# Kernel tuning notes

Measured on AMD Instinct MI355X. Metric: run time of the kernel, lower is better.

## Reference

```python
import jax, jax.numpy as jnp
import numpy as np

NUM_HEADS = 8

def setup_inputs() -> dict:
    key = jax.random.key(0)
    k0, k1, k2, k3 = jax.random.split(key, 4)
    B, C, H, W = 2, 512, 64, 64
    x = jax.random.normal(k0, (B, C, H, W), dtype=jnp.float32)
    # binary ROI mask (hard mode): 1 inside region, 0 outside
    mask = (jax.random.uniform(k1, (B, 1, H, W)) > 0.5).astype(jnp.float32)
    Wqkv = jax.random.normal(k2, (3 * C, C), dtype=jnp.float32) * 0.02
    bqkv = jnp.zeros((3 * C,), dtype=jnp.float32)
    Wproj = jax.random.normal(k3, (C, C), dtype=jnp.float32) * 0.02
    bproj = jnp.zeros((C,), dtype=jnp.float32)
    return {"x": x, "mask": mask, "Wqkv": Wqkv, "bqkv": bqkv, "Wproj": Wproj, "bproj": bproj}


def reference(x, mask, Wqkv, bqkv, Wproj, bproj):
    B, C, H, W = x.shape
    N = H * W
    d = C // NUM_HEADS
    scale = d ** (-0.5)

    xf = x.reshape(B, C, N)
    # 1x1 conv == per-pixel linear: [3C,C] @ [B,C,N]
    qkv = jnp.einsum('oc,bcn->bon', Wqkv, xf) + bqkv[None, :, None]
    q, k, v = jnp.split(qkv, 3, axis=1)  # each [B,C,N]

    def to_heads(t):  # [B,C,N] -> [B,h,N,d]
        return t.reshape(B, NUM_HEADS, d, N).transpose(0, 1, 3, 2)

    q, k, v = to_heads(q), to_heads(k), to_heads(v)

    attn = jnp.einsum('bhnd,bhmd->bhnm', q, k) * scale  # [B,h,N,N]
    # hard mask bias: -10000 on keys outside ROI, broadcast over query dim
    roi = mask.reshape(B, 1, 1, N)
    attn = attn + (1.0 - roi) * (-10000.0)
    attn = jax.nn.softmax(attn, axis=-1)
    # attn_drop = 0.0 -> identity

    out = jnp.einsum('bhnm,bhmd->bhnd', attn, v)  # [B,h,N,d]
    out = out.transpose(0, 1, 3, 2).reshape(B, C, N)
    out = jnp.einsum('oc,bcn->bon', Wproj, out) + bproj[None, :, None]
    return out.reshape(B, C, H, W)
```

## Files before the change

### kernel.cpp

```cpp
#include <hip/hip_runtime.h>

#define BB 2
#define CC 512
#define NH 8
#define DDIM 64
#define NN 4096
#define QSCALE 0.18033688011112042f
#define MBIAS  -14426.950408889634f

typedef __bf16 bfx8 __attribute__((ext_vector_type(8)));
typedef __bf16 bf2  __attribute__((ext_vector_type(2)));
typedef float  f32x4 __attribute__((ext_vector_type(4)));
typedef int    i32x4 __attribute__((ext_vector_type(4)));
typedef ushort usx8  __attribute__((ext_vector_type(8)));

__device__ inline ushort f2bf(float f) {
  return __builtin_bit_cast(ushort, (__bf16)f);
}
__device__ inline float bf2f(ushort u) {
  return (float)__builtin_bit_cast(__bf16, u);
}

__device__ __forceinline__ void gload_lds16(const void* g, void* l) {
  __builtin_amdgcn_global_load_lds(
      (const __attribute__((address_space(1))) void*)g,
      (__attribute__((address_space(3))) void*)l, 16, 0, 0);
}

__device__ __forceinline__ void swap32(int& a, int& b) {
  asm("v_permlane32_swap_b32 %0, %1" : "+v"(a), "+v"(b));
}
__device__ __forceinline__ void swap16(int& a, int& b) {
  asm("v_permlane16_swap_b32 %0, %1" : "+v"(a), "+v"(b));
}

__global__ __launch_bounds__(256)
void convert_w(const float* __restrict__ Wqkv, const float* __restrict__ Wproj,
               ushort* __restrict__ Wq, ushort* __restrict__ Wp) {
    const int n1 = (1536*CC)/4;
    const int n2 = (CC*CC)/4;
    int i = blockIdx.x*256 + threadIdx.x;
    if (i < n1) {
        float4 v = *(const float4*)(&Wqkv[(size_t)i*4]);
        if (i < 65536) { v.x*=QSCALE; v.y*=QSCALE; v.z*=QSCALE; v.w*=QSCALE; }
        ushort4 o; o.x=f2bf(v.x); o.y=f2bf(v.y); o.z=f2bf(v.z); o.w=f2bf(v.w);
        *(ushort4*)(&Wq[(size_t)i*4]) = o;
    } else if (i < n1+n2) {
        int j = i - n1;
        float4 v = *(const float4*)(&Wproj[(size_t)j*4]);
        ushort4 o; o.x=f2bf(v.x); o.y=f2bf(v.y); o.z=f2bf(v.z); o.w=f2bf(v.w);
        *(ushort4*)(&Wp[(size_t)j*4]) = o;
    }
}

__global__ __launch_bounds__(256)
void transpose_x(const float* __restrict__ x, ushort* __restrict__ xT) {
    const int bn = blockIdx.x, bc = blockIdx.y, b = blockIdx.z;
    const int t = threadIdx.x;
    __shared__ float T[64][65];
    const int n0 = bn*64, c0 = bc*64;
    const int tc = t >> 4, tn4 = (t & 15) * 4;
    #pragma unroll
    for (int r = 0; r < 4; ++r) {
        int c = tc + r*16;
        float4 v = *(const float4*)(&x[((size_t)b*CC + c0 + c)*NN + n0 + tn4]);
        T[c][tn4+0] = v.x; T[c][tn4+1] = v.y; T[c][tn4+2] = v.z; T[c][tn4+3] = v.w;
    }
    __syncthreads();
    #pragma unroll
    for (int r = 0; r < 4; ++r) {
        int n = tc + r*16;
        ushort4 o;
        o.x = f2bf(T[tn4+0][n]); o.y = f2bf(T[tn4+1][n]);
        o.z = f2bf(T[tn4+2][n]); o.w = f2bf(T[tn4+3][n]);
        *(ushort4*)(&xT[((size_t)b*NN + n0 + n)*CC + c0 + tn4]) = o;
    }
}

__global__ __launch_bounds__(256)
void qkv_mfma(const ushort* __restrict__ xT, const ushort* __restrict__ Wb,
              const float* __restrict__ bias, ushort* __restrict__ qws,
              ushort* __restrict__ kws, ushort* __restrict__ vws) {
    const int bn = blockIdx.x;
    const int bo = blockIdx.y;
    const int b  = blockIdx.z;
    const int t  = threadIdx.x;
    const int w  = t >> 6, l = t & 63, g = l >> 4, m = l & 15;
    const int o0 = bo * 128, n0 = bn * 128;
    const int part = o0 >> 9;
    const int wr = w >> 1, wc = w & 1;

    __shared__ __align__(16) ushort SH[2*128*64];
    ushort* Xs  = SH;
    ushort* Ws_ = SH + 128*64;

    const ushort* xbase = xT + ((size_t)b*NN + n0)*CC;
    const ushort* wbase = Wb + (size_t)o0*CC;

    f32x4 acc[4][4];
    #pragma unroll
    for (int i=0;i<4;i++)
        #pragma unroll
        for (int j=0;j<4;j++) acc[i][j] = (f32x4){0.f,0.f,0.f,0.f};

    const ushort* R = (part < 2) ? Xs  : Ws_;
    const ushort* Cc = (part < 2) ? Ws_ : Xs;

    for (int k0 = 0; k0 < CC; k0 += 64) {
        #pragma unroll
        for (int it = 0; it < 4; ++it) {
            int c16 = (it*4 + w)*64 + l;
            int row = c16 >> 3;
            int gch = (c16 & 7) ^ (row & 7);
            gload_lds16(xbase + (size_t)row*CC + k0 + gch*8, Xs  + c16*8);
            gload_lds16(wbase + (size_t)row*CC + k0 + gch*8, Ws_ + c16*8);
        }
        __syncthreads();
        __builtin_amdgcn_s_setprio(1);
        #pragma unroll
        for (int kc = 0; kc < 2; ++kc) {
            bfx8 ra[4], cb[4];
            #pragma unroll
            for (int f = 0; f < 4; ++f) {
                int rrow = wr*64 + f*16 + m;
                ra[f] = *(const bfx8*)(R  + (rrow*8 + ((kc*4+g) ^ (rrow&7)))*8);
                int crow = wc*64 + f*16 + m;
                cb[f] = *(const bfx8*)(Cc + (crow*8 + ((kc*4+g) ^ (crow&7)))*8);
            }
            #pragma unroll
            for (int i = 0; i < 4; ++i)
                #pragma unroll
                for (int j = 0; j < 4; ++j)
                    acc[i][j] = __builtin_amdgcn_mfma_f32_16x16x32_bf16(ra[i], cb[j], acc[i][j], 0, 0, 0);
        }
        __builtin_amdgcn_s_setprio(0);
        __syncthreads();
    }

    float bvj[4];
    float bvi[4][4];
    if (part < 2) {
        const float bs = (part == 0) ? QSCALE : 1.f;
        #pragma unroll
        for (int j = 0; j < 4; ++j) bvj[j] = bias[o0 + wc*64 + j*16 + m] * bs;
    } else {
        #pragma unroll
        for (int i = 0; i < 4; ++i) {
            const float4 bt = *(const float4*)(&bias[o0 + wr*64 + i*16 + g*4]);
            bvi[i][0]=bt.x; bvi[i][1]=bt.y; bvi[i][2]=bt.z; bvi[i][3]=bt.w;
        }
    }
    ushort* Lb = SH;
    #pragma unroll
    for (int i = 0; i < 4; ++i)
        #pragma unroll
        for (int j = 0; j < 4; ++j)
            #pragma unroll
            for (int r = 0; r < 4; ++r) {
                int A = wr*64 + i*16 + g*4 + r;
                int Bc = wc*64 + j*16 + m;
                float val = acc[i][j][r] + ((part < 2) ? bvj[j] : bvi[i][r]);
                int ch = (Bc >> 3) ^ (A & 15);
                Lb[A*128 + ch*8 + (Bc & 7)] = f2bf(val);
            }
    __syncthreads();
    {
        const int row = t >> 1, cp = t & 1;
        const int h0 = (o0 & 511) >> 6;
        ushort* dp;
        if (part < 2) {
            ushort* dst = (part == 0) ? qws : kws;
            dp = dst + (((size_t)b*NH + h0 + cp)*NN + n0 + row)*DDIM;
        } else {
            int h = h0 + (row >> 6), d = row & 63;
            dp = vws + (((size_t)b*NH + h)*DDIM + d)*NN + n0 + cp*64;
        }
        #pragma unroll
        for (int k = 0; k < 8; ++k) {
            int ch = (cp*8 + k) ^ (row & 15);
            *(float4*)(dp + k*8) = *(const float4*)(&Lb[row*128 + ch*8]);
        }
    }
}

__global__ __launch_bounds__(256, 4)
void attn_mfma(const ushort* __restrict__ qw, const ushort* __restrict__ kw,
               const ushort* __restrict__ vw, const float* __restrict__ mask,
               ushort* __restrict__ opart, float* __restrict__ lpart) {
    const int qt = blockIdx.x >> 1, half = blockIdx.x & 1;
    const int h = blockIdx.y, b = blockIdx.z;
    const int t = threadIdx.x;
    const int w = t >> 6, l = t & 63, g = l >> 4, m = l & 15;
    const int n0 = qt * 128;
    const int koff0 = half * 2048;
    const size_t bh = (size_t)b * NH + h;
    const ushort* qp = qw + bh * (size_t)NN * DDIM;
    const ushort* kp = kw + bh * (size_t)NN * DDIM;
    const ushort* vp = vw + bh * (size_t)DDIM * NN;

    __shared__ __align__(16) ushort Ks[2][64*64];
    __shared__ __align__(16) ushort Vs[2][64*64];
    __shared__ float mb[2][64];

    #define STAGE(buf, ko) { \
        _Pragma("unroll") \
        for (int it = 0; it < 2; ++it) { \
            int c16 = it*256 + t; \
            int row = c16 >> 3, gch = (c16 & 7) ^ (row & 7); \
            gload_lds16(kp + (size_t)((ko) + row)*DDIM + gch*8, &Ks[buf][c16*8]); \
            gload_lds16(vp + (size_t)row*NN + (ko) + gch*8, &Vs[buf][c16*8]); \
        } }

    bfx8 qf[2][2];
    #pragma unroll
    for (int qi = 0; qi < 2; ++qi)
        #pragma unroll
        for (int kc = 0; kc < 2; ++kc)
            qf[qi][kc] = *(const bfx8*)(qp + (size_t)(n0 + w*32 + qi*16 + m)*DDIM + kc*32 + g*8);

    f32x4 o[2][4];
    #pragma unroll
    for (int qi=0; qi<2; ++qi)
        #pragma unroll
        for (int f=0; f<4; ++f) o[qi][f] = (f32x4){0.f,0.f,0.f,0.f};
    float l_part[2] = {0.f, 0.f};

    STAGE(0, koff0);
    float mreg = 0.f;
    if (t < 64) mreg = mask[(size_t)b*NN + koff0 + t];
    if (t < 64) mb[0][t] = (1.f - mreg) * MBIAS;
    if (t < 64) mreg = mask[(size_t)b*NN + koff0 + 64 + t];
    __syncthreads();

    for (int kt = 0; kt < 32; ++kt) {
        const int cur = kt & 1, nxt = cur ^ 1;
        if (kt + 1 < 32) {
            STAGE(nxt, koff0 + (kt+1)*64);
            if (t < 64) mb[nxt][t] = (1.f - mreg) * MBIAS;
            if (kt + 2 < 32 && t < 64) mreg = mask[(size_t)b*NN + koff0 + (kt+2)*64 + t];
        }

        float4 mbv[4];
        #pragma unroll
        for (int f=0; f<4; ++f) mbv[f] = *(const float4*)(&mb[cur][f*16 + 4*g]);

        f32x4 sa[2][4];
        #pragma unroll
        for (int qi=0; qi<2; ++qi)
            #pragma unroll
            for (int f=0; f<4; ++f)
                sa[qi][f] = (f32x4){mbv[f].x, mbv[f].y, mbv[f].z, mbv[f].w};
        __builtin_amdgcn_s_setprio(1);
        #pragma unroll
        for (int kc=0; kc<2; ++kc)
            #pragma unroll
            for (int f=0; f<4; ++f) {
                int row = f*16 + m;
                bfx8 kf = *(const bfx8*)(&Ks[cur][row*64 + ((kc*32 + g*8) ^ ((row&7)*8))]);
                #pragma unroll
                for (int qi=0; qi<2; ++qi)
                    sa[qi][f] = __builtin_amdgcn_mfma_f32_16x16x32_bf16(kf, qf[qi][kc], sa[qi][f], 0, 0, 0);
            }
        __builtin_amdgcn_s_setprio(0);

        bfx8 pa[2][2];
        #pragma unroll
        for (int qi=0; qi<2; ++qi) {
            float pv_[4][4];
            float tsum = 0.f;
            #pragma unroll
            for (int f=0; f<4; ++f)
                #pragma unroll
                for (int r=0; r<4; ++r) {
                    float p = __builtin_amdgcn_exp2f(sa[qi][f][r]);
                    pv_[f][r] = p;
                    tsum += p;
                }
            l_part[qi] += tsum;

            int u[4][2];
            #pragma unroll
            for (int f=0; f<4; ++f)
                #pragma unroll
                for (int pp=0; pp<2; ++pp) {
                    bf2 tpk = { (__bf16)pv_[f][2*pp], (__bf16)pv_[f][2*pp+1] };
                    u[f][pp] = __builtin_bit_cast(int, tpk);
                }
            #pragma unroll
            for (int pp=0; pp<2; ++pp) { swap32(u[0][pp], u[1][pp]); swap32(u[2][pp], u[3][pp]); }
            #pragma unroll
            for (int pp=0; pp<2; ++pp) { swap16(u[0][pp], u[1][pp]); swap16(u[2][pp], u[3][pp]); }
            pa[qi][0] = __builtin_bit_cast(bfx8, (i32x4){u[0][0], u[0][1], u[1][0], u[1][1]});
            pa[qi][1] = __builtin_bit_cast(bfx8, (i32x4){u[2][0], u[2][1], u[3][0], u[3][1]});
        }

        __builtin_amdgcn_s_setprio(1);
        #pragma unroll
        for (int kc=0; kc<2; ++kc)
            #pragma unroll
            for (int f=0; f<4; ++f) {
                int row = f*16 + m;
                bfx8 vf = *(const bfx8*)(&Vs[cur][row*64 + ((kc*32 + g*8) ^ ((row&7)*8))]);
                #pragma unroll
                for (int qi=0; qi<2; ++qi)
                    o[qi][f] = __builtin_amdgcn_mfma_f32_16x16x32_bf16(pa[qi][kc], vf, o[qi][f], 0, 0, 0);
            }
        __builtin_amdgcn_s_setprio(0);
        __syncthreads();
    }

    const size_t obase = (bh*2 + half) * (size_t)NN;
    #pragma unroll
    for (int qi=0; qi<2; ++qi) {
        float l_tot = l_part[qi] + __shfl_xor(l_part[qi], 16);
        l_tot += __shfl_xor(l_tot, 32);
        if (g == 0) lpart[obase + n0 + w*32 + qi*16 + m] = l_tot;
        #pragma unroll
        for (int f=0; f<4; ++f)
            #pragma unroll
            for (int r=0; r<4; ++r)
                opart[(obase + n0 + w*32 + qi*16 + 4*g + r)*DDIM + f*16 + m] = f2bf(o[qi][f][r]);
    }
    #undef STAGE
}

__global__ __launch_bounds__(256)
void combine_k(const ushort* __restrict__ opart, const float* __restrict__ lpart,
               ushort* __restrict__ aob) {
    const int t = threadIdx.x;
    const int n = blockIdx.x*64 + (t >> 2), dq = t & 3;
    const int h = blockIdx.y, b = blockIdx.z;
    const size_t bh = (size_t)b*NH + h;
    const float linv = 1.f / (lpart[(bh*2+0)*NN + n] + lpart[(bh*2+1)*NN + n]);
    const ushort* p0 = opart + ((bh*2+0)*(size_t)NN + n)*DDIM + dq*16;
    const ushort* p1 = opart + ((bh*2+1)*(size_t)NN + n)*DDIM + dq*16;
    ushort* dst = aob + ((size_t)b*NN + n)*CC + h*DDIM + dq*16;
    #pragma unroll
    for (int c = 0; c < 2; ++c) {
        usx8 u0 = *(const usx8*)(p0 + c*8);
        usx8 u1 = *(const usx8*)(p1 + c*8);
        usx8 res;
        #pragma unroll
        for (int j = 0; j < 8; ++j)
            res[j] = f2bf((bf2f(u0[j]) + bf2f(u1[j])) * linv);
        *(usx8*)(dst + c*8) = res;
    }
}

__global__ __launch_bounds__(256)
void proj_mfma(const ushort* __restrict__ aob, const ushort* __restrict__ Wp,
               const float* __restrict__ bias, float* __restrict__ out) {
    const int bn = blockIdx.x;
    const int bo = blockIdx.y;
    const int b  = blockIdx.z;
    const int t  = threadIdx.x;
    const int w  = t >> 6, l = t & 63, g = l >> 4, m = l & 15;
    const int o0 = bo * 128, n0 = bn * 128;
    const int wr = w >> 1, wc = w & 1;

    __shared__ __align__(16) ushort As_[128*64];
    __shared__ __align__(16) ushort Ws_[128*64];

    const ushort* abase = aob + ((size_t)b*NN + n0)*CC;
    const ushort* wbase = Wp + (size_t)o0*CC;

    f32x4 acc[4][4];
    #pragma unroll
    for (int i=0;i<4;i++)
        #pragma unroll
        for (int j=0;j<4;j++) acc[i][j] = (f32x4){0.f,0.f,0.f,0.f};

    for (int k0 = 0; k0 < CC; k0 += 64) {
        #pragma unroll
        for (int it = 0; it < 4; ++it) {
            int c16 = (it*4 + w)*64 + l;
            int row = c16 >> 3;
            int gch = (c16 & 7) ^ (row & 7);
            gload_lds16(abase + (size_t)row*CC + k0 + gch*8, As_ + c16*8);
            gload_lds16(wbase + (size_t)row*CC + k0 + gch*8, Ws_ + c16*8);
        }
        __syncthreads();
        __builtin_amdgcn_s_setprio(1);
        #pragma unroll
        for (int kc = 0; kc < 2; ++kc) {
            bfx8 ra[4], cb[4];
            #pragma unroll
            for (int f = 0; f < 4; ++f) {
                int rrow = wr*64 + f*16 + m;
                ra[f] = *(const bfx8*)(Ws_ + (rrow*8 + ((kc*4+g) ^ (rrow&7)))*8);
                int crow = wc*64 + f*16 + m;
                cb[f] = *(const bfx8*)(As_ + (crow*8 + ((kc*4+g) ^ (crow&7)))*8);
            }
            #pragma unroll
            for (int i = 0; i < 4; ++i)
                #pragma unroll
                for (int j = 0; j < 4; ++j)
                    acc[i][j] = __builtin_amdgcn_mfma_f32_16x16x32_bf16(ra[i], cb[j], acc[i][j], 0, 0, 0);
        }
        __builtin_amdgcn_s_setprio(0);
        __syncthreads();
    }
    #pragma unroll
    for (int i = 0; i < 4; ++i)
        #pragma unroll
        for (int r = 0; r < 4; ++r) {
            int o = o0 + wr*64 + i*16 + g*4 + r;
            float bv = bias[o];
            float* dp = out + ((size_t)b*CC + o)*NN;
            #pragma unroll
            for (int j = 0; j < 4; ++j) {
                int n = n0 + wc*64 + j*16 + m;
                dp[n] = acc[i][j][r] + bv;
            }
        }
}

extern "C" void kernel_launch(void* const* d_in, const int* in_sizes, int n_in,
                              void* d_out, int out_size, void* d_ws, size_t ws_size,
                              hipStream_t stream) {
    const float* x     = (const float*)d_in[0];
    const float* mask  = (const float*)d_in[1];
    const float* Wqkv  = (const float*)d_in[2];
    const float* bqkv  = (const float*)d_in[3];
    const float* Wproj = (const float*)d_in[4];
    const float* bproj = (const float*)d_in[5];
    float* out = (float*)d_out;

    const size_t per = (size_t)BB*NH*NN*DDIM;
    ushort* qws = (ushort*)d_ws;
    ushort* kws = qws + per;
    ushort* vws = kws + per;
    ushort* xTb = vws + per;
    ushort* aob = xTb + per;
    ushort* Wqb = aob + per;
    ushort* Wpb = Wqb + (size_t)1536*CC;
    ushort* opart = Wpb + (size_t)CC*CC;
    float*  lpart = (float*)(opart + 2*per);

    convert_w<<<dim3(1024), 256, 0, stream>>>(Wqkv, Wproj, Wqb, Wpb);
    transpose_x<<<dim3(64, 8, BB), 256, 0, stream>>>(x, xTb);
    qkv_mfma<<<dim3(32, 12, BB), 256, 0, stream>>>(xTb, Wqb, bqkv, qws, kws, vws);
    attn_mfma<<<dim3(64, NH, BB), 256, 0, stream>>>(qws, kws, vws, mask, opart, lpart);
    combine_k<<<dim3(64, NH, BB), 256, 0, stream>>>(opart, lpart, aob);
    proj_mfma<<<dim3(32, 4, BB), 256, 0, stream>>>(aob, Wpb, bproj, out);
}
```

Before: 201.7 us.

## Double-buffer GEMM loads, remap blocks across XCDs, precompute mask bias, MFMA row sums

The QKV and projection GEMMs now double-buffer their LDS tiles so the next K-slice loads while the current one computes. All three GEMM-style kernels use a 1D grid with an XCD-aware block remap, which groups blocks that share data onto the same chiplet for L2 reuse. The mask bias is precomputed once in the weight-conversion kernel and read directly from global memory, removing the LDS mask staging. The softmax denominator is now accumulated with an extra MFMA against a ones vector instead of scalar adds and shuffles. The costs are doubled LDS use in the GEMMs, which may lower occupancy, and extra MFMA work in the attention kernel.

```diff
diff --git a/kernel.cpp b/kernel.cpp
--- a/kernel.cpp
+++ b/kernel.cpp
@@ -36,9 +36,12 @@
 
 __global__ __launch_bounds__(256)
 void convert_w(const float* __restrict__ Wqkv, const float* __restrict__ Wproj,
-               ushort* __restrict__ Wq, ushort* __restrict__ Wp) {
+               const float* __restrict__ mask,
+               ushort* __restrict__ Wq, ushort* __restrict__ Wp,
+               float* __restrict__ mbias) {
     const int n1 = (1536*CC)/4;
     const int n2 = (CC*CC)/4;
+    const int n3 = (BB*NN)/4;
     int i = blockIdx.x*256 + threadIdx.x;
     if (i < n1) {
         float4 v = *(const float4*)(&Wqkv[(size_t)i*4]);
@@ -50,6 +53,13 @@
         float4 v = *(const float4*)(&Wproj[(size_t)j*4]);
         ushort4 o; o.x=f2bf(v.x); o.y=f2bf(v.y); o.z=f2bf(v.z); o.w=f2bf(v.w);
         *(ushort4*)(&Wp[(size_t)j*4]) = o;
+    } else if (i < n1+n2+n3) {
+        int j = i - n1 - n2;
+        float4 mv = *(const float4*)(&mask[(size_t)j*4]);
+        float4 ob;
+        ob.x = (1.f - mv.x) * MBIAS; ob.y = (1.f - mv.y) * MBIAS;
+        ob.z = (1.f - mv.z) * MBIAS; ob.w = (1.f - mv.w) * MBIAS;
+        *(float4*)(&mbias[(size_t)j*4]) = ob;
     }
 }
 
@@ -81,18 +91,17 @@
 void qkv_mfma(const ushort* __restrict__ xT, const ushort* __restrict__ Wb,
               const float* __restrict__ bias, ushort* __restrict__ qws,
               ushort* __restrict__ kws, ushort* __restrict__ vws) {
-    const int bn = blockIdx.x;
-    const int bo = blockIdx.y;
-    const int b  = blockIdx.z;
+    const int wg = (blockIdx.x & 7) * 96 + (blockIdx.x >> 3);
+    const int bn = wg & 31;
+    const int bo = (wg % 384) / 32;
+    const int b  = wg / 384;
     const int t  = threadIdx.x;
     const int w  = t >> 6, l = t & 63, g = l >> 4, m = l & 15;
     const int o0 = bo * 128, n0 = bn * 128;
     const int part = o0 >> 9;
     const int wr = w >> 1, wc = w & 1;
 
-    __shared__ __align__(16) ushort SH[2*128*64];
-    ushort* Xs  = SH;
-    ushort* Ws_ = SH + 128*64;
+    __shared__ __align__(16) ushort SH[4*128*64];
 
     const ushort* xbase = xT + ((size_t)b*NN + n0)*CC;
     const ushort* wbase = Wb + (size_t)o0*CC;
@@ -103,19 +112,28 @@
         #pragma unroll
         for (int j=0;j<4;j++) acc[i][j] = (f32x4){0.f,0.f,0.f,0.f};
 
-    const ushort* R = (part < 2) ? Xs  : Ws_;
-    const ushort* Cc = (part < 2) ? Ws_ : Xs;
-
-    for (int k0 = 0; k0 < CC; k0 += 64) {
-        #pragma unroll
-        for (int it = 0; it < 4; ++it) {
-            int c16 = (it*4 + w)*64 + l;
-            int row = c16 >> 3;
-            int gch = (c16 & 7) ^ (row & 7);
-            gload_lds16(xbase + (size_t)row*CC + k0 + gch*8, Xs  + c16*8);
-            gload_lds16(wbase + (size_t)row*CC + k0 + gch*8, Ws_ + c16*8);
-        }
-        __syncthreads();
+    #define QSTAGE(buf, k0) { \
+        _Pragma("unroll") \
+        for (int it = 0; it < 4; ++it) { \
+            int c16 = (it*4 + w)*64 + l; \
+            int row = c16 >> 3; \
+            int gch = (c16 & 7) ^ (row & 7); \
+            gload_lds16(xbase + (size_t)row*CC + (k0) + gch*8, SH + (buf)*8192 + c16*8); \
+            gload_lds16(wbase + (size_t)row*CC + (k0) + gch*8, SH + 16384 + (buf)*8192 + c16*8); \
+        } }
+
+    QSTAGE(0, 0);
+    __syncthreads();
+
+    for (int k0i = 0; k0i < 8; ++k0i) {
+        const int cur = k0i & 1, nxt = cur ^ 1;
+        if (k0i + 1 < 8) QSTAGE(nxt, (k0i+1)*64);
+
+        const ushort* Xs  = SH + cur*8192;
+        const ushort* Ws_ = SH + 16384 + cur*8192;
+        const ushort* R  = (part < 2) ? Xs  : Ws_;
+        const ushort* Cc = (part < 2) ? Ws_ : Xs;
+
         __builtin_amdgcn_s_setprio(1);
         #pragma unroll
         for (int kc = 0; kc < 2; ++kc) {
@@ -136,6 +154,7 @@
         __builtin_amdgcn_s_setprio(0);
         __syncthreads();
     }
+    #undef QSTAGE
 
     float bvj[4];
     float bvi[4][4];
@@ -185,10 +204,11 @@
 
 __global__ __launch_bounds__(256, 4)
 void attn_mfma(const ushort* __restrict__ qw, const ushort* __restrict__ kw,
-               const ushort* __restrict__ vw, const float* __restrict__ mask,
+               const ushort* __restrict__ vw, const float* __restrict__ mbias,
                ushort* __restrict__ opart, float* __restrict__ lpart) {
-    const int qt = blockIdx.x >> 1, half = blockIdx.x & 1;
-    const int h = blockIdx.y, b = blockIdx.z;
+    const int wg = (blockIdx.x & 7) * 128 + (blockIdx.x >> 3);
+    const int qt = (wg & 63) >> 1, half = wg & 1;
+    const int h = (wg >> 6) & 7, b = wg >> 9;
     const int t = threadIdx.x;
     const int w = t >> 6, l = t & 63, g = l >> 4, m = l & 15;
     const int n0 = qt * 128;
@@ -197,10 +217,10 @@
     const ushort* qp = qw + bh * (size_t)NN * DDIM;
     const ushort* kp = kw + bh * (size_t)NN * DDIM;
     const ushort* vp = vw + bh * (size_t)DDIM * NN;
+    const float*  mbp = mbias + (size_t)b*NN + koff0;
 
     __shared__ __align__(16) ushort Ks[2][64*64];
     __shared__ __align__(16) ushort Vs[2][64*64];
-    __shared__ float mb[2][64];
 
     #define STAGE(buf, ko) { \
         _Pragma("unroll") \
@@ -223,33 +243,31 @@
     for (int qi=0; qi<2; ++qi)
         #pragma unroll
         for (int f=0; f<4; ++f) o[qi][f] = (f32x4){0.f,0.f,0.f,0.f};
-    float l_part[2] = {0.f, 0.f};
+    f32x4 lacc[2];
+    lacc[0] = (f32x4){0.f,0.f,0.f,0.f};
+    lacc[1] = (f32x4){0.f,0.f,0.f,0.f};
+    const bfx8 vones = {(__bf16)1.f,(__bf16)1.f,(__bf16)1.f,(__bf16)1.f,
+                        (__bf16)1.f,(__bf16)1.f,(__bf16)1.f,(__bf16)1.f};
 
     STAGE(0, koff0);
-    float mreg = 0.f;
-    if (t < 64) mreg = mask[(size_t)b*NN + koff0 + t];
-    if (t < 64) mb[0][t] = (1.f - mreg) * MBIAS;
-    if (t < 64) mreg = mask[(size_t)b*NN + koff0 + 64 + t];
     __syncthreads();
 
     for (int kt = 0; kt < 32; ++kt) {
         const int cur = kt & 1, nxt = cur ^ 1;
-        if (kt + 1 < 32) {
-            STAGE(nxt, koff0 + (kt+1)*64);
-            if (t < 64) mb[nxt][t] = (1.f - mreg) * MBIAS;
-            if (kt + 2 < 32 && t < 64) mreg = mask[(size_t)b*NN + koff0 + (kt+2)*64 + t];
-        }
-
-        float4 mbv[4];
-        #pragma unroll
-        for (int f=0; f<4; ++f) mbv[f] = *(const float4*)(&mb[cur][f*16 + 4*g]);
+
+        float4 mb4[4];
+        #pragma unroll
+        for (int f=0; f<4; ++f)
+            mb4[f] = *(const float4*)(mbp + kt*64 + f*16 + 4*g);
+
+        if (kt + 1 < 32) STAGE(nxt, koff0 + (kt+1)*64);
 
         f32x4 sa[2][4];
         #pragma unroll
         for (int qi=0; qi<2; ++qi)
             #pragma unroll
             for (int f=0; f<4; ++f)
-                sa[qi][f] = (f32x4){mbv[f].x, mbv[f].y, mbv[f].z, mbv[f].w};
+                sa[qi][f] = __builtin_bit_cast(f32x4, mb4[f]);
         __builtin_amdgcn_s_setprio(1);
         #pragma unroll
         for (int kc=0; kc<2; ++kc)
@@ -267,16 +285,11 @@
         #pragma unroll
         for (int qi=0; qi<2; ++qi) {
             float pv_[4][4];
-            float tsum = 0.f;
             #pragma unroll
             for (int f=0; f<4; ++f)
                 #pragma unroll
-                for (int r=0; r<4; ++r) {
-                    float p = __builtin_amdgcn_exp2f(sa[qi][f][r]);
-                    pv_[f][r] = p;
-                    tsum += p;
-                }
-            l_part[qi] += tsum;
+                for (int r=0; r<4; ++r)
+                    pv_[f][r] = __builtin_amdgcn_exp2f(sa[qi][f][r]);
 
             int u[4][2];
             #pragma unroll
@@ -296,7 +309,7 @@
 
         __builtin_amdgcn_s_setprio(1);
         #pragma unroll
-        for (int kc=0; kc<2; ++kc)
+        for (int kc=0; kc<2; ++kc) {
             #pragma unroll
             for (int f=0; f<4; ++f) {
                 int row = f*16 + m;
@@ -305,23 +318,29 @@
                 for (int qi=0; qi<2; ++qi)
                     o[qi][f] = __builtin_amdgcn_mfma_f32_16x16x32_bf16(pa[qi][kc], vf, o[qi][f], 0, 0, 0);
             }
+            #pragma unroll
+            for (int qi=0; qi<2; ++qi)
+                lacc[qi] = __builtin_amdgcn_mfma_f32_16x16x32_bf16(pa[qi][kc], vones, lacc[qi], 0, 0, 0);
+        }
         __builtin_amdgcn_s_setprio(0);
         __syncthreads();
     }
+    #undef STAGE
 
     const size_t obase = (bh*2 + half) * (size_t)NN;
     #pragma unroll
     for (int qi=0; qi<2; ++qi) {
-        float l_tot = l_part[qi] + __shfl_xor(l_part[qi], 16);
-        l_tot += __shfl_xor(l_tot, 32);
-        if (g == 0) lpart[obase + n0 + w*32 + qi*16 + m] = l_tot;
+        if (m == 0) {
+            #pragma unroll
+            for (int r=0; r<4; ++r)
+                lpart[obase + n0 + w*32 + qi*16 + 4*g + r] = lacc[qi][r];
+        }
         #pragma unroll
         for (int f=0; f<4; ++f)
             #pragma unroll
             for (int r=0; r<4; ++r)
                 opart[(obase + n0 + w*32 + qi*16 + 4*g + r)*DDIM + f*16 + m] = f2bf(o[qi][f][r]);
     }
-    #undef STAGE
 }
 
 __global__ __launch_bounds__(256)
@@ -350,16 +369,16 @@
 __global__ __launch_bounds__(256)
 void proj_mfma(const ushort* __restrict__ aob, const ushort* __restrict__ Wp,
                const float* __restrict__ bias, float* __restrict__ out) {
-    const int bn = blockIdx.x;
-    const int bo = blockIdx.y;
-    const int b  = blockIdx.z;
+    const int wg = (blockIdx.x & 7) * 32 + (blockIdx.x >> 3);
+    const int bn = wg & 31;
+    const int bo = (wg >> 5) & 3;
+    const int b  = wg >> 7;
     const int t  = threadIdx.x;
     const int w  = t >> 6, l = t & 63, g = l >> 4, m = l & 15;
     const int o0 = bo * 128, n0 = bn * 128;
     const int wr = w >> 1, wc = w & 1;
 
-    __shared__ __align__(16) ushort As_[128*64];
-    __shared__ __align__(16) ushort Ws_[128*64];
+    __shared__ __align__(16) ushort SH[4*128*64];
 
     const ushort* abase = aob + ((size_t)b*NN + n0)*CC;
     const ushort* wbase = Wp + (size_t)o0*CC;
@@ -370,16 +389,26 @@
         #pragma unroll
         for (int j=0;j<4;j++) acc[i][j] = (f32x4){0.f,0.f,0.f,0.f};
 
-    for (int k0 = 0; k0 < CC; k0 += 64) {
-        #pragma unroll
-        for (int it = 0; it < 4; ++it) {
-            int c16 = (it*4 + w)*64 + l;
-            int row = c16 >> 3;
-            int gch = (c16 & 7) ^ (row & 7);
-            gload_lds16(abase + (size_t)row*CC + k0 + gch*8, As_ + c16*8);
-            gload_lds16(wbase + (size_t)row*CC + k0 + gch*8, Ws_ + c16*8);
-        }
-        __syncthreads();
+    #define PSTAGE(buf, k0) { \
+        _Pragma("unroll") \
+        for (int it = 0; it < 4; ++it) { \
+            int c16 = (it*4 + w)*64 + l; \
+            int row = c16 >> 3; \
+            int gch = (c16 & 7) ^ (row & 7); \
+            gload_lds16(abase + (size_t)row*CC + (k0) + gch*8, SH + (buf)*8192 + c16*8); \
+            gload_lds16(wbase + (size_t)row*CC + (k0) + gch*8, SH + 16384 + (buf)*8192 + c16*8); \
+        } }
+
+    PSTAGE(0, 0);
+    __syncthreads();
+
+    for (int k0i = 0; k0i < 8; ++k0i) {
+        const int cur = k0i & 1, nxt = cur ^ 1;
+        if (k0i + 1 < 8) PSTAGE(nxt, (k0i+1)*64);
+
+        const ushort* As_ = SH + cur*8192;
+        const ushort* Ws_ = SH + 16384 + cur*8192;
+
         __builtin_amdgcn_s_setprio(1);
         #pragma unroll
         for (int kc = 0; kc < 2; ++kc) {
@@ -400,6 +429,8 @@
         __builtin_amdgcn_s_setprio(0);
         __syncthreads();
     }
+    #undef PSTAGE
+
     #pragma unroll
     for (int i = 0; i < 4; ++i)
         #pragma unroll
@@ -436,11 +467,12 @@
     ushort* Wpb = Wqb + (size_t)1536*CC;
     ushort* opart = Wpb + (size_t)CC*CC;
     float*  lpart = (float*)(opart + 2*per);
-
-    convert_w<<<dim3(1024), 256, 0, stream>>>(Wqkv, Wproj, Wqb, Wpb);
+    float*  mbias = lpart + (size_t)BB*NH*2*NN;
+
+    convert_w<<<dim3(1032), 256, 0, stream>>>(Wqkv, Wproj, mask, Wqb, Wpb, mbias);
     transpose_x<<<dim3(64, 8, BB), 256, 0, stream>>>(x, xTb);
-    qkv_mfma<<<dim3(32, 12, BB), 256, 0, stream>>>(xTb, Wqb, bqkv, qws, kws, vws);
-    attn_mfma<<<dim3(64, NH, BB), 256, 0, stream>>>(qws, kws, vws, mask, opart, lpart);
+    qkv_mfma<<<dim3(768), 256, 0, stream>>>(xTb, Wqb, bqkv, qws, kws, vws);
+    attn_mfma<<<dim3(1024), 256, 0, stream>>>(qws, kws, vws, mbias, opart, lpart);
     combine_k<<<dim3(64, NH, BB), 256, 0, stream>>>(opart, lpart, aob);
-    proj_mfma<<<dim3(32, 4, BB), 256, 0, stream>>>(aob, Wpb, bproj, out);
-}
+    proj_mfma<<<dim3(256), 256, 0, stream>>>(aob, Wpb, bproj, out);
+}
```

Result: faster. 196.6 us (-2.5%).
